# Performance work log

Measured on AMD Instinct MI355X. Metric: run time of the kernel, lower is better.

The kernel has to match this reference:

```python
import jax, jax.numpy as jnp
import numpy as np

N = 8192
X_DIM = 256
Y_DIM = 256


def setup_inputs() -> dict:
    key = jax.random.key(0)
    kx, ky, kw = jax.random.split(key, 3)
    x_samples = jax.random.normal(kx, (N, X_DIM), dtype=jnp.float32)
    y_samples = jax.random.normal(ky, (N, Y_DIM), dtype=jnp.float32)
    # kaiming-uniform-ish init for the bilinear weight [x_dim, y_dim]
    bound = float(np.sqrt(6.0 / X_DIM))
    w = jax.random.uniform(kw, (X_DIM, Y_DIM), dtype=jnp.float32,
                           minval=-bound, maxval=bound)
    return {"x_samples": x_samples, "y_samples": y_samples, "w": w}


def reference(x_samples, y_samples, w):
    # Pairwise bilinear scores S[i, b] = x[i] @ W @ y[b]
    # (equivalent to the original's tiled einsum, without O(N^2*dim) tiles)
    n = y_samples.shape[0]
    xw = x_samples @ w                      # [N, y_dim]
    S = xw @ y_samples.T                    # [N, N], S[i, b]
    # T0[i] = S[i, i]; T1.logsumexp(dim=1)[b] = logsumexp_i S[i, b]
    t0_mean = jnp.mean(jnp.diagonal(S))
    lse_mean = jnp.mean(jax.nn.logsumexp(S, axis=0))
    lower_bound = t0_mean - (lse_mean - jnp.log(jnp.float32(n)))
    return lower_bound
```

## Files before the change

### kernel.cpp

```cpp
#include <hip/hip_runtime.h>

typedef __attribute__((ext_vector_type(8))) short bf16x8;
typedef __attribute__((ext_vector_type(4))) float f32x4;

__device__ __forceinline__ unsigned short f2bf(float f) {
    unsigned int u = __float_as_uint(f);
    u += 0x7fffu + ((u >> 16) & 1u);
    return (unsigned short)(u >> 16);
}

__global__ void cast_wy_kernel(const float* __restrict__ y, const float* __restrict__ w,
                               unsigned short* __restrict__ YB, unsigned short* __restrict__ WT,
                               float* __restrict__ scal)
{
    int idx = blockIdx.x * 256 + threadIdx.x;
    const float4 yv = ((const float4*)y)[idx];
    ushort4 b;
    b.x = f2bf(yv.x); b.y = f2bf(yv.y); b.z = f2bf(yv.z); b.w = f2bf(yv.w);
    ((ushort4*)YB)[idx] = b;
    if (idx < 16384) {
        const float4 wv = ((const float4*)w)[idx];
        int k = idx >> 6;
        int n0 = (idx & 63) * 4;
        WT[(size_t)(n0 + 0) * 256 + k] = f2bf(wv.x);
        WT[(size_t)(n0 + 1) * 256 + k] = f2bf(wv.y);
        WT[(size_t)(n0 + 2) * 256 + k] = f2bf(wv.z);
        WT[(size_t)(n0 + 3) * 256 + k] = f2bf(wv.w);
    }
    if (idx == 0) {
        scal[0] = 0.f; scal[1] = 0.f;
        ((unsigned int*)scal)[2] = 0u;
    }
}

__global__ __launch_bounds__(256, 2)
void gemm0_kernel(const float* __restrict__ X, const unsigned short* __restrict__ WT,
                  unsigned short* __restrict__ XWB)
{
    __shared__ __align__(16) unsigned short As[128 * 64];
    __shared__ __align__(16) unsigned short Bs[128 * 64];

    const int tid  = threadIdx.x;
    const int lane = tid & 63;
    const int w    = tid >> 6;
    const int wm   = w >> 1, wn = w & 1;
    const int frow = lane & 15, quad = lane >> 4;
    const int rowBase = blockIdx.y * 128;
    const int colBase = blockIdx.x * 128;

    int aOff[4][2], bOff[4][2];
#pragma unroll
    for (int mi = 0; mi < 4; ++mi)
#pragma unroll
        for (int kk = 0; kk < 2; ++kk) {
            int ka = kk * 4 + quad;
            int ra = wm * 64 + mi * 16 + frow;
            aOff[mi][kk] = ra * 64 + ((ka ^ (ra & 7)) << 3);
            int rb = wn * 64 + mi * 16 + frow;
            bOff[mi][kk] = rb * 64 + ((ka ^ (rb & 7)) << 3);
        }

    f32x4 acc[4][4];
#pragma unroll
    for (int i = 0; i < 4; ++i)
#pragma unroll
        for (int j = 0; j < 4; ++j)
            acc[i][j] = f32x4{0.f, 0.f, 0.f, 0.f};

#pragma unroll
    for (int kt = 0; kt < 4; ++kt) {
        const int k0 = kt * 64;
#pragma unroll
        for (int it = 0; it < 4; ++it) {
            int p  = it * 256 + tid;
            int r  = p >> 3;
            int s  = p & 7;
            int kc = s ^ (r & 7);
            const unsigned short* gb = WT + (size_t)(colBase + r) * 256 + k0 + (kc << 3);
            __builtin_amdgcn_global_load_lds(
                (const __attribute__((address_space(1))) void*)gb,
                (__attribute__((address_space(3))) void*)&Bs[p << 3], 16, 0, 0);
        }
#pragma unroll
        for (int it = 0; it < 8; ++it) {
            int fidx = it * 256 + tid;
            int r  = fidx >> 4;
            int c4 = fidx & 15;
            float4 v = *(const float4*)&X[(size_t)(rowBase + r) * 256 + k0 + c4 * 4];
            ushort4 u;
            u.x = f2bf(v.x); u.y = f2bf(v.y); u.z = f2bf(v.z); u.w = f2bf(v.w);
            int slot = (c4 >> 1) ^ (r & 7);
            *(ushort4*)&As[r * 64 + (slot << 3) + (c4 & 1) * 4] = u;
        }
        __syncthreads();
#pragma unroll
        for (int kk = 0; kk < 2; ++kk) {
            bf16x8 a[4], b[4];
#pragma unroll
            for (int mi = 0; mi < 4; ++mi) a[mi] = *(const bf16x8*)&As[aOff[mi][kk]];
#pragma unroll
            for (int ni = 0; ni < 4; ++ni) b[ni] = *(const bf16x8*)&Bs[bOff[ni][kk]];
#pragma unroll
            for (int mi = 0; mi < 4; ++mi)
#pragma unroll
                for (int ni = 0; ni < 4; ++ni)
                    acc[mi][ni] = __builtin_amdgcn_mfma_f32_16x16x32_bf16(
                        a[mi], b[ni], acc[mi][ni], 0, 0, 0);
        }
        __syncthreads();
    }

#pragma unroll
    for (int mi = 0; mi < 4; ++mi)
#pragma unroll
        for (int ni = 0; ni < 4; ++ni)
#pragma unroll
            for (int r2 = 0; r2 < 4; ++r2) {
                int row = rowBase + wm * 64 + mi * 16 + quad * 4 + r2;
                int col = colBase + wn * 64 + ni * 16 + frow;
                XWB[(size_t)row * 256 + col] = f2bf(acc[mi][ni][r2]);
            }
}

__global__ __launch_bounds__(256, 3)
void gemm1_kernel(const unsigned short* __restrict__ A,
                  const unsigned short* __restrict__ B,
                  float* __restrict__ P, float* __restrict__ scal)
{
    __shared__ __align__(16) unsigned short As[128 * 64];
    __shared__ __align__(16) unsigned short Bs[128 * 64];
    __shared__ float lsebuf[256];

    const int tid  = threadIdx.x;
    const int lane = tid & 63;
    const int w    = tid >> 6;
    const int wm   = w >> 1, wn = w & 1;
    const int frow = lane & 15, quad = lane >> 4;
    const int rowBase = blockIdx.y * 128;
    const int colBase = blockIdx.x * 128;

    int aOff[4][2], bOff[4][2];
#pragma unroll
    for (int mi = 0; mi < 4; ++mi)
#pragma unroll
        for (int kk = 0; kk < 2; ++kk) {
            int ka = kk * 4 + quad;
            int ra = wm * 64 + mi * 16 + frow;
            aOff[mi][kk] = ra * 64 + ((ka ^ (ra & 7)) << 3);
            int rb = wn * 64 + mi * 16 + frow;
            bOff[mi][kk] = rb * 64 + ((ka ^ (rb & 7)) << 3);
        }

    f32x4 acc[4][4];
#pragma unroll
    for (int i = 0; i < 4; ++i)
#pragma unroll
        for (int j = 0; j < 4; ++j)
            acc[i][j] = f32x4{0.f, 0.f, 0.f, 0.f};

#pragma unroll
    for (int kt = 0; kt < 4; ++kt) {
        const int k0 = kt * 64;
#pragma unroll
        for (int it = 0; it < 4; ++it) {
            int p  = it * 256 + tid;
            int r  = p >> 3;
            int s  = p & 7;
            int kc = s ^ (r & 7);
            const unsigned short* ga = A + (size_t)(rowBase + r) * 256 + k0 + (kc << 3);
            const unsigned short* gb = B + (size_t)(colBase + r) * 256 + k0 + (kc << 3);
            __builtin_amdgcn_global_load_lds(
                (const __attribute__((address_space(1))) void*)ga,
                (__attribute__((address_space(3))) void*)&As[p << 3], 16, 0, 0);
            __builtin_amdgcn_global_load_lds(
                (const __attribute__((address_space(1))) void*)gb,
                (__attribute__((address_space(3))) void*)&Bs[p << 3], 16, 0, 0);
        }
        __syncthreads();
#pragma unroll
        for (int kk = 0; kk < 2; ++kk) {
            bf16x8 a[4], b[4];
#pragma unroll
            for (int mi = 0; mi < 4; ++mi) a[mi] = *(const bf16x8*)&As[aOff[mi][kk]];
#pragma unroll
            for (int ni = 0; ni < 4; ++ni) b[ni] = *(const bf16x8*)&Bs[bOff[ni][kk]];
#pragma unroll
            for (int mi = 0; mi < 4; ++mi)
#pragma unroll
                for (int ni = 0; ni < 4; ++ni)
                    acc[mi][ni] = __builtin_amdgcn_mfma_f32_16x16x32_bf16(
                        a[mi], b[ni], acc[mi][ni], 0, 0, 0);
        }
        __syncthreads();
    }

#pragma unroll
    for (int ni = 0; ni < 4; ++ni) {
        float m = -1e30f;
#pragma unroll
        for (int mi = 0; mi < 4; ++mi)
#pragma unroll
            for (int r2 = 0; r2 < 4; ++r2) m = fmaxf(m, acc[mi][ni][r2]);
        m = fmaxf(m, __shfl_xor(m, 16));
        m = fmaxf(m, __shfl_xor(m, 32));
        float ssum = 0.f;
#pragma unroll
        for (int mi = 0; mi < 4; ++mi)
#pragma unroll
            for (int r2 = 0; r2 < 4; ++r2) ssum += __expf(acc[mi][ni][r2] - m);
        ssum += __shfl_xor(ssum, 16);
        ssum += __shfl_xor(ssum, 32);
        if (quad == 0)
            lsebuf[wm * 128 + wn * 64 + ni * 16 + frow] = m + __logf(ssum);
    }
    if (blockIdx.x == blockIdx.y && wm == wn) {
        float v = 0.f;
#pragma unroll
        for (int mi = 0; mi < 4; ++mi)
#pragma unroll
            for (int r2 = 0; r2 < 4; ++r2)
                if (quad * 4 + r2 == frow) v += acc[mi][mi][r2];
#pragma unroll
        for (int o = 1; o < 64; o <<= 1) v += __shfl_xor(v, o);
        if (lane == 0) atomicAdd(&scal[0], v);
    }
    __syncthreads();
    if (tid < 128) {
        float a = lsebuf[tid], b = lsebuf[128 + tid];
        float mm = fmaxf(a, b);
        P[(size_t)blockIdx.y * 8192 + colBase + tid]
            = mm + __logf(__expf(a - mm) + __expf(b - mm));
    }
}

__global__ void combine_kernel(const float* __restrict__ P, float* __restrict__ scal,
                               float* __restrict__ out)
{
    __shared__ float red[256];
    const int tid = threadIdx.x;
    const int col = blockIdx.x * 256 + tid;
    float m = -1e30f, s = 0.f;
#pragma unroll 8
    for (int j = 0; j < 64; ++j) {
        float v = P[(size_t)j * 8192 + col];
        float nm = fmaxf(m, v);
        s = s * __expf(m - nm) + __expf(v - nm);
        m = nm;
    }
    red[tid] = m + logf(s);
    __syncthreads();
#pragma unroll
    for (int o = 128; o > 0; o >>= 1) {
        if (tid < o) red[tid] += red[tid + o];
        __syncthreads();
    }
    if (tid == 0) {
        atomicAdd(&scal[1], red[0]);
        __threadfence();
        unsigned int old = __hip_atomic_fetch_add((unsigned int*)&scal[2], 1u,
                                                  __ATOMIC_ACQ_REL, __HIP_MEMORY_SCOPE_AGENT);
        if (old == 31u) {
            float t0 = __hip_atomic_load(&scal[0], __ATOMIC_RELAXED, __HIP_MEMORY_SCOPE_AGENT);
            float ls = __hip_atomic_load(&scal[1], __ATOMIC_RELAXED, __HIP_MEMORY_SCOPE_AGENT);
            const float invN = 1.f / 8192.f;
            out[0] = t0 * invN - (ls * invN - logf(8192.f));
        }
    }
}

extern "C" void kernel_launch(void* const* d_in, const int* in_sizes, int n_in,
                              void* d_out, int out_size, void* d_ws, size_t ws_size,
                              hipStream_t stream)
{
    const float* x = (const float*)d_in[0];
    const float* y = (const float*)d_in[1];
    const float* w = (const float*)d_in[2];
    float* out = (float*)d_out;

    char* ws = (char*)d_ws;
    unsigned short* YB  = (unsigned short*)(ws);
    unsigned short* XWB = (unsigned short*)(ws + 0x400000);
    unsigned short* WT  = (unsigned short*)(ws + 0x800000);
    float*          P   = (float*)        (ws + 0x820000);
    float*          scal= (float*)        (ws + 0xA20000);

    cast_wy_kernel<<<2048, 256, 0, stream>>>(y, w, YB, WT, scal);
    gemm0_kernel<<<dim3(2, 64), 256, 0, stream>>>(x, WT, XWB);
    gemm1_kernel<<<dim3(64, 64), 256, 0, stream>>>(XWB, YB, P, scal);
    combine_kernel<<<32, 256, 0, stream>>>(P, scal, out);
}
```

Baseline: 123.4 us.

## Quantize XW and Y to fp8 and use scaled fp8 MFMA for pairwise GEMM

Y and the XW intermediate are now stored as fp8 instead of bf16. The NxN score GEMM uses the MI355 16x16x128 f8f6f4 scaled MFMA with unit scales. The whole K=256 tile is loaded into LDS in one pass with a 16-byte XOR swizzle, which removes the per-K-step barriers. This halves operand bandwidth and doubles MFMA throughput, but it raises LDS use (64KB), lowers occupancy to 2, and adds fp8 quantization error to the logsumexp result.

After: 114.0 us. 7.7% less time.

```diff
diff --git a/kernel.cpp b/kernel.cpp
--- a/kernel.cpp
+++ b/kernel.cpp
@@ -2,6 +2,10 @@
 
 typedef __attribute__((ext_vector_type(8))) short bf16x8;
 typedef __attribute__((ext_vector_type(4))) float f32x4;
+typedef __attribute__((ext_vector_type(8))) int   i32x8;
+typedef __attribute__((ext_vector_type(4))) int   i32x4;
+
+union OpU { i32x8 v; i32x4 h[2]; };
 
 __device__ __forceinline__ unsigned short f2bf(float f) {
     unsigned int u = __float_as_uint(f);
@@ -10,14 +14,14 @@
 }
 
 __global__ void cast_wy_kernel(const float* __restrict__ y, const float* __restrict__ w,
-                               unsigned short* __restrict__ YB, unsigned short* __restrict__ WT,
+                               unsigned char* __restrict__ YQ, unsigned short* __restrict__ WT,
                                float* __restrict__ scal)
 {
     int idx = blockIdx.x * 256 + threadIdx.x;
     const float4 yv = ((const float4*)y)[idx];
-    ushort4 b;
-    b.x = f2bf(yv.x); b.y = f2bf(yv.y); b.z = f2bf(yv.z); b.w = f2bf(yv.w);
-    ((ushort4*)YB)[idx] = b;
+    int pk = __builtin_amdgcn_cvt_pk_fp8_f32(yv.x, yv.y, 0, 0);
+    pk     = __builtin_amdgcn_cvt_pk_fp8_f32(yv.z, yv.w, pk, 1);
+    ((int*)YQ)[idx] = pk;
     if (idx < 16384) {
         const float4 wv = ((const float4*)w)[idx];
         int k = idx >> 6;
@@ -35,7 +39,7 @@
 
 __global__ __launch_bounds__(256, 2)
 void gemm0_kernel(const float* __restrict__ X, const unsigned short* __restrict__ WT,
-                  unsigned short* __restrict__ XWB)
+                  unsigned char* __restrict__ XWQ)
 {
     __shared__ __align__(16) unsigned short As[128 * 64];
     __shared__ __align__(16) unsigned short Bs[128 * 64];
@@ -118,18 +122,20 @@
             for (int r2 = 0; r2 < 4; ++r2) {
                 int row = rowBase + wm * 64 + mi * 16 + quad * 4 + r2;
                 int col = colBase + wn * 64 + ni * 16 + frow;
-                XWB[(size_t)row * 256 + col] = f2bf(acc[mi][ni][r2]);
+                float v = acc[mi][ni][r2];
+                int q = __builtin_amdgcn_cvt_pk_fp8_f32(v, v, 0, 0);
+                XWQ[(size_t)row * 256 + col] = (unsigned char)(q & 0xff);
             }
 }
 
-__global__ __launch_bounds__(256, 3)
-void gemm1_kernel(const unsigned short* __restrict__ A,
-                  const unsigned short* __restrict__ B,
+__global__ __launch_bounds__(256, 2)
+void gemm1_kernel(const unsigned char* __restrict__ A,
+                  const unsigned char* __restrict__ B,
                   float* __restrict__ P, float* __restrict__ scal)
 {
-    __shared__ __align__(16) unsigned short As[128 * 64];
-    __shared__ __align__(16) unsigned short Bs[128 * 64];
-    __shared__ float lsebuf[256];
+    __shared__ __align__(16) unsigned char As[128 * 256];
+    __shared__ __align__(16) unsigned char Bs[128 * 256];
+    float* lsebuf = (float*)As;
 
     const int tid  = threadIdx.x;
     const int lane = tid & 63;
@@ -139,17 +145,22 @@
     const int rowBase = blockIdx.y * 128;
     const int colBase = blockIdx.x * 128;
 
-    int aOff[4][2], bOff[4][2];
-#pragma unroll
-    for (int mi = 0; mi < 4; ++mi)
-#pragma unroll
-        for (int kk = 0; kk < 2; ++kk) {
-            int ka = kk * 4 + quad;
-            int ra = wm * 64 + mi * 16 + frow;
-            aOff[mi][kk] = ra * 64 + ((ka ^ (ra & 7)) << 3);
-            int rb = wn * 64 + mi * 16 + frow;
-            bOff[mi][kk] = rb * 64 + ((ka ^ (rb & 7)) << 3);
-        }
+#pragma unroll
+    for (int it = 0; it < 8; ++it) {
+        int p  = it * 256 + tid;
+        int r  = p >> 4;
+        int s  = p & 15;
+        int kc = s ^ (r & 15);
+        const unsigned char* ga = A + (size_t)(rowBase + r) * 256 + (kc << 4);
+        const unsigned char* gb = B + (size_t)(colBase + r) * 256 + (kc << 4);
+        __builtin_amdgcn_global_load_lds(
+            (const __attribute__((address_space(1))) void*)ga,
+            (__attribute__((address_space(3))) void*)&As[p << 4], 16, 0, 0);
+        __builtin_amdgcn_global_load_lds(
+            (const __attribute__((address_space(1))) void*)gb,
+            (__attribute__((address_space(3))) void*)&Bs[p << 4], 16, 0, 0);
+    }
+    __syncthreads();
 
     f32x4 acc[4][4];
 #pragma unroll
@@ -159,40 +170,37 @@
             acc[i][j] = f32x4{0.f, 0.f, 0.f, 0.f};
 
 #pragma unroll
-    for (int kt = 0; kt < 4; ++kt) {
-        const int k0 = kt * 64;
-#pragma unroll
-        for (int it = 0; it < 4; ++it) {
-            int p  = it * 256 + tid;
-            int r  = p >> 3;
-            int s  = p & 7;
-            int kc = s ^ (r & 7);
-            const unsigned short* ga = A + (size_t)(rowBase + r) * 256 + k0 + (kc << 3);
-            const unsigned short* gb = B + (size_t)(colBase + r) * 256 + k0 + (kc << 3);
-            __builtin_amdgcn_global_load_lds(
-                (const __attribute__((address_space(1))) void*)ga,
-                (__attribute__((address_space(3))) void*)&As[p << 3], 16, 0, 0);
-            __builtin_amdgcn_global_load_lds(
-                (const __attribute__((address_space(1))) void*)gb,
-                (__attribute__((address_space(3))) void*)&Bs[p << 3], 16, 0, 0);
-        }
-        __syncthreads();
-#pragma unroll
-        for (int kk = 0; kk < 2; ++kk) {
-            bf16x8 a[4], b[4];
-#pragma unroll
-            for (int mi = 0; mi < 4; ++mi) a[mi] = *(const bf16x8*)&As[aOff[mi][kk]];
-#pragma unroll
-            for (int ni = 0; ni < 4; ++ni) b[ni] = *(const bf16x8*)&Bs[bOff[ni][kk]];
-#pragma unroll
-            for (int mi = 0; mi < 4; ++mi)
-#pragma unroll
-                for (int ni = 0; ni < 4; ++ni)
-                    acc[mi][ni] = __builtin_amdgcn_mfma_f32_16x16x32_bf16(
-                        a[mi], b[ni], acc[mi][ni], 0, 0, 0);
-        }
-        __syncthreads();
-    }
+    for (int kk = 0; kk < 2; ++kk) {
+        const int c0 = kk * 8 + quad * 2;
+        i32x8 a[4], b[4];
+#pragma unroll
+        for (int mi = 0; mi < 4; ++mi) {
+            int ra = wm * 64 + mi * 16 + frow;
+            OpU u;
+            u.h[0] = *(const i32x4*)&As[ra * 256 + ((c0 ^ frow) << 4)];
+            u.h[1] = *(const i32x4*)&As[ra * 256 + (((c0 + 1) ^ frow) << 4)];
+            a[mi] = u.v;
+        }
+#pragma unroll
+        for (int ni = 0; ni < 4; ++ni) {
+            int rb = wn * 64 + ni * 16 + frow;
+            OpU u;
+            u.h[0] = *(const i32x4*)&Bs[rb * 256 + ((c0 ^ frow) << 4)];
+            u.h[1] = *(const i32x4*)&Bs[rb * 256 + (((c0 + 1) ^ frow) << 4)];
+            b[ni] = u.v;
+        }
+#pragma unroll
+        for (int mi = 0; mi < 4; ++mi)
+#pragma unroll
+            for (int ni = 0; ni < 4; ++ni)
+                acc[mi][ni] = __builtin_amdgcn_mfma_scale_f32_16x16x128_f8f6f4(
+                    a[mi], b[ni], acc[mi][ni],
+                    0, 0,
+                    0, 0x7f7f7f7f,
+                    0, 0x7f7f7f7f);
+    }
+
+    __syncthreads();
 
 #pragma unroll
     for (int ni = 0; ni < 4; ++ni) {
@@ -278,14 +286,14 @@
     float* out = (float*)d_out;
 
     char* ws = (char*)d_ws;
-    unsigned short* YB  = (unsigned short*)(ws);
-    unsigned short* XWB = (unsigned short*)(ws + 0x400000);
-    unsigned short* WT  = (unsigned short*)(ws + 0x800000);
-    float*          P   = (float*)        (ws + 0x820000);
-    float*          scal= (float*)        (ws + 0xA20000);
-
-    cast_wy_kernel<<<2048, 256, 0, stream>>>(y, w, YB, WT, scal);
-    gemm0_kernel<<<dim3(2, 64), 256, 0, stream>>>(x, WT, XWB);
-    gemm1_kernel<<<dim3(64, 64), 256, 0, stream>>>(XWB, YB, P, scal);
+    unsigned char*  YQ  = (unsigned char*)(ws);
+    unsigned char*  XWQ = (unsigned char*)(ws + 0x200000);
+    unsigned short* WT  = (unsigned short*)(ws + 0x400000);
+    float*          P   = (float*)        (ws + 0x420000);
+    float*          scal= (float*)        (ws + 0x620000);
+
+    cast_wy_kernel<<<2048, 256, 0, stream>>>(y, w, YQ, WT, scal);
+    gemm0_kernel<<<dim3(2, 64), 256, 0, stream>>>(x, WT, XWQ);
+    gemm1_kernel<<<dim3(64, 64), 256, 0, stream>>>(XWQ, YQ, P, scal);
     combine_kernel<<<32, 256, 0, stream>>>(P, scal, out);
 }
```
